# Performance work log

Hardware: AMD Instinct MI355X
Metric: run time of the kernel (lower is better)

## Reference

```python
import jax, jax.numpy as jnp
import numpy as np

N_ADDR = 400000
N_TX = 400000
E = 1500000
F_IN = 64
HID = 32
OUT = 2


def _sage(x_src, x_dst, ei, Wl, bl, Wr, n_dst):
    # SAGEConv: mean-aggregate source feats over incoming edges, then
    # out = lin_l(agg) + lin_r(x_dst). Nodes with no in-edges get agg=0.
    src, dst = ei[0], ei[1]
    msg = x_src[src]                                            # [E, F]
    s = jax.ops.segment_sum(msg, dst, num_segments=n_dst)       # [N_dst, F]
    cnt = jax.ops.segment_sum(jnp.ones((ei.shape[1], 1), x_src.dtype), dst,
                              num_segments=n_dst)               # [N_dst, 1]
    agg = s / jnp.maximum(cnt, 1.0)
    return agg @ Wl + bl + x_dst @ Wr


def setup_inputs() -> dict:
    key = jax.random.key(0)
    ks = jax.random.split(key, 24)
    d = {}
    d['x_addr'] = jax.random.normal(ks[0], (N_ADDR, F_IN), jnp.float32)
    d['x_tx'] = jax.random.normal(ks[1], (N_TX, F_IN), jnp.float32)
    d['ei_at'] = jax.random.randint(ks[2], (2, E), 0, N_ADDR)   # addr->tx (src idx < N_ADDR, dst idx < N_TX)
    d['ei_ta'] = jax.random.randint(ks[3], (2, E), 0, N_TX)     # tx->addr
    def w(k, i, o):
        return jax.random.normal(k, (i, o), jnp.float32) * (1.0 / np.sqrt(i))
    d['w1_tx_l'] = w(ks[4], F_IN, HID); d['b1_tx'] = jnp.zeros((HID,), jnp.float32)
    d['w1_tx_r'] = w(ks[5], F_IN, HID)
    d['w1_ad_l'] = w(ks[6], F_IN, HID); d['b1_ad'] = jnp.zeros((HID,), jnp.float32)
    d['w1_ad_r'] = w(ks[7], F_IN, HID)
    d['w2_tx_l'] = w(ks[8], HID, HID); d['b2_tx'] = jnp.zeros((HID,), jnp.float32)
    d['w2_tx_r'] = w(ks[9], HID, HID)
    d['w2_ad_l'] = w(ks[10], HID, HID); d['b2_ad'] = jnp.zeros((HID,), jnp.float32)
    d['w2_ad_r'] = w(ks[11], HID, HID)
    d['w3_tx_l'] = w(ks[12], HID, HID); d['b3_tx'] = jnp.zeros((HID,), jnp.float32)
    d['w3_tx_r'] = w(ks[13], HID, HID)
    d['w3_ad_l'] = w(ks[14], HID, HID); d['b3_ad'] = jnp.zeros((HID,), jnp.float32)
    d['w3_ad_r'] = w(ks[15], HID, HID)
    d['w_out'] = w(ks[16], HID, OUT); d['b_out'] = jnp.zeros((OUT,), jnp.float32)
    return d


def reference(x_addr, x_tx, ei_at, ei_ta,
              w1_tx_l, b1_tx, w1_tx_r, w1_ad_l, b1_ad, w1_ad_r,
              w2_tx_l, b2_tx, w2_tx_r, w2_ad_l, b2_ad, w2_ad_r,
              w3_tx_l, b3_tx, w3_tx_r, w3_ad_l, b3_ad, w3_ad_r,
              w_out, b_out):
    # Layer 1 (both node types updated simultaneously from previous x_dict)
    tx = jax.nn.relu(_sage(x_addr, x_tx, ei_at, w1_tx_l, b1_tx, w1_tx_r, N_TX))
    ad = jax.nn.relu(_sage(x_tx, x_addr, ei_ta, w1_ad_l, b1_ad, w1_ad_r, N_ADDR))
    # Layer 2
    tx2 = jax.nn.relu(_sage(ad, tx, ei_at, w2_tx_l, b2_tx, w2_tx_r, N_TX))
    ad2 = jax.nn.relu(_sage(tx, ad, ei_ta, w2_ad_l, b2_ad, w2_ad_r, N_ADDR))
    # Layer 3
    ad3 = jax.nn.relu(_sage(tx2, ad2, ei_ta, w3_ad_l, b3_ad, w3_ad_r, N_ADDR))
    # Final classifier on 'addr' nodes (dropout is identity at inference)
    return ad3 @ w_out + b_out
```

## Files before the change

### kernel.cpp

```cpp
#include <hip/hip_runtime.h>

#define NADDR 400000
#define NTX   400000
#define NEDGE 1500000
#define FIN   64
#define HID   32
#define NB    1563
#define LSTR  36

static inline int cdiv_host(long a, int b) { return (int)((a + b - 1) / b); }


__global__ void k_hist(const int* __restrict__ at_dst, const int* __restrict__ ta_dst,
                       int* __restrict__ bcnt , int GH) {
    __shared__ int h[NB];
    bool wh = blockIdx.x >= GH;
    int blk = blockIdx.x - (wh ? GH : 0);
    const int* dst = wh ? ta_dst : at_dst;
    for (int i = threadIdx.x; i < NB; i += 256) h[i] = 0;
    __syncthreads();
    for (long e = (long)blk * 256 + threadIdx.x; e < NEDGE; e += (long)GH * 256)
        atomicAdd(&h[dst[e] >> 8], 1);
    __syncthreads();
    int* g = bcnt + (wh ? NB : 0);
    for (int i = threadIdx.x; i < NB; i += 256) {
        int v = h[i];
        if (v) atomicAdd(&g[i], v);
    }
}

__global__ void k_scan_nb(const int* __restrict__ bcnt, int* __restrict__ bbase,
                          int* __restrict__ gcur) {
    __shared__ int sm[256];
    __shared__ int carry;
    int w = blockIdx.x;
    int t = threadIdx.x;
    if (t == 0) carry = 0;
    __syncthreads();
    for (int base = 0; base < NB; base += 256) {
        int i = base + t;
        int v = (i < NB) ? bcnt[w * NB + i] : 0;
        sm[t] = v;
        __syncthreads();
        for (int off = 1; off < 256; off <<= 1) {
            int x = (t >= off) ? sm[t - off] : 0;
            __syncthreads();
            sm[t] += x;
            __syncthreads();
        }
        int excl = sm[t] - v + carry;
        if (i < NB) { bbase[w * (NB + 1) + i] = excl; gcur[w * NB + i] = excl; }
        int tot = sm[255];
        __syncthreads();
        if (t == 0) carry += tot;
        __syncthreads();
    }
    if (t == 0) bbase[w * (NB + 1) + NB] = NEDGE;
}

__global__ void k_dist(const int* __restrict__ ei_at, const int* __restrict__ ei_ta,
                       int* __restrict__ gcur, unsigned* __restrict__ eb_at,
                       unsigned* __restrict__ eb_ta, int GD) {
    __shared__ int h[NB];
    __shared__ int bs[NB];
    bool wh = blockIdx.x >= GD;
    int blk = blockIdx.x - (wh ? GD : 0);
    const int* ei = wh ? ei_ta : ei_at;
    unsigned* eb = wh ? eb_ta : eb_at;
    for (int i = threadIdx.x; i < NB; i += 256) h[i] = 0;
    __syncthreads();
    long e0 = (long)blk * 256 + threadIdx.x;
    long stride = (long)GD * 256;
    for (long e = e0; e < NEDGE; e += stride)
        atomicAdd(&h[ei[NEDGE + e] >> 8], 1);
    __syncthreads();
    int* gc = gcur + (wh ? NB : 0);
    for (int i = threadIdx.x; i < NB; i += 256) {
        int c = h[i];
        bs[i] = c ? atomicAdd(&gc[i], c) : 0;
        h[i] = 0;
    }
    __syncthreads();
    for (long e = e0; e < NEDGE; e += stride) {
        int d = ei[NEDGE + e];
        int s = ei[e];
        int b = d >> 8;
        int r = atomicAdd(&h[b], 1);
        eb[bs[b] + r] = ((unsigned)s << 8) | (unsigned)(d & 255);
    }
}

__global__ void k_csrb(const unsigned* __restrict__ eb_at, const unsigned* __restrict__ eb_ta,
                       const int* __restrict__ bbase,
                       int* __restrict__ rp_tx, int* __restrict__ rp_ad,
                       int* __restrict__ col_at, int* __restrict__ col_ta) {
    __shared__ int deg[256];
    __shared__ int cur[256];
    __shared__ int sm[256];
    bool wh = blockIdx.x >= NB;
    int b = blockIdx.x - (wh ? NB : 0);
    const unsigned* eb = wh ? eb_ta : eb_at;
    int* rp  = wh ? rp_ad  : rp_tx;
    int* col = wh ? col_ta : col_at;
    const int* bb = bbase + (wh ? (NB + 1) : 0);
    int e0 = bb[b], e1 = bb[b + 1];
    int t = threadIdx.x;
    deg[t] = 0;
    __syncthreads();
    for (int e = e0 + t; e < e1; e += 256)
        atomicAdd(&deg[eb[e] & 255], 1);
    __syncthreads();
    int v = deg[t];
    sm[t] = v;
    __syncthreads();
    for (int off = 1; off < 256; off <<= 1) {
        int x = (t >= off) ? sm[t - off] : 0;
        __syncthreads();
        sm[t] += x;
        __syncthreads();
    }
    int excl = sm[t] - v;
    int node = b * 256 + t;
    if (node < 400000) rp[node] = e0 + excl;
    cur[t] = e0 + excl;
    __syncthreads();
    for (int e = e0 + t; e < e1; e += 256) {
        unsigned p = eb[e];
        int idx = atomicAdd(&cur[p & 255], 1);
        col[idx] = (int)(p >> 8);
    }
    if (t == 0 && b == 0) rp[400000] = NEDGE;
}

template<int F, bool DUAL>
__global__ __launch_bounds__(256)
void k_pre(const float* __restrict__ x,
           const float* __restrict__ wa, const float* __restrict__ ba,
           float* __restrict__ outa,
           const float* __restrict__ wb, const float* __restrict__ bb,
           float* __restrict__ outb, int n) {
    __shared__ alignas(16) float xs[256 * LSTR];
    int t = threadIdx.x;
    long row0 = (long)blockIdx.x * 256;

    float aa[HID], ab[DUAL ? HID : 1];
#pragma unroll
    for (int j = 0; j < HID; ++j) aa[j] = ba ? ba[j] : 0.0f;
    if (DUAL) {
#pragma unroll
        for (int j = 0; j < HID; ++j) ab[j] = bb[j];
    }

    for (int kt = 0; kt < F / 32; ++kt) {
#pragma unroll
        for (int sub = 0; sub < 8; ++sub) {
            int f = sub * 256 + t;
            int r = f >> 3, k4 = f & 7;
            long gr = row0 + r;
            if (gr >= n) gr = n - 1;
            float4 v = *(const float4*)(x + gr * F + kt * 32 + k4 * 4);
            *(float4*)(&xs[r * LSTR + k4 * 4]) = v;
        }
        __syncthreads();
        float xr[32];
#pragma unroll
        for (int q = 0; q < 8; ++q) {
            float4 v = *(const float4*)(&xs[t * LSTR + q * 4]);
            xr[q * 4 + 0] = v.x; xr[q * 4 + 1] = v.y;
            xr[q * 4 + 2] = v.z; xr[q * 4 + 3] = v.w;
        }
        const float* wka = wa + kt * 32 * HID;
#pragma unroll
        for (int k = 0; k < 32; ++k) {
            float xk = xr[k];
            const float* wr = wka + k * HID;
#pragma unroll
            for (int j = 0; j < HID; ++j) aa[j] = __builtin_fmaf(xk, wr[j], aa[j]);
        }
        if (DUAL) {
            const float* wkb = wb + kt * 32 * HID;
#pragma unroll
            for (int k = 0; k < 32; ++k) {
                float xk = xr[k];
                const float* wr = wkb + k * HID;
#pragma unroll
                for (int j = 0; j < HID; ++j) ab[j] = __builtin_fmaf(xk, wr[j], ab[j]);
            }
        }
        __syncthreads();
    }

#pragma unroll
    for (int j = 0; j < HID; j += 4)
        *(float4*)(&xs[t * LSTR + j]) = make_float4(aa[j], aa[j + 1], aa[j + 2], aa[j + 3]);
    __syncthreads();
#pragma unroll
    for (int sub = 0; sub < 8; ++sub) {
        int f = sub * 256 + t;
        int r = f >> 3, k4 = f & 7;
        long gr = row0 + r;
        if (gr < n) {
            float4 v = *(const float4*)(&xs[r * LSTR + k4 * 4]);
            *(float4*)(outa + gr * HID + k4 * 4) = v;
        }
    }
    if (DUAL) {
        __syncthreads();
#pragma unroll
        for (int j = 0; j < HID; j += 4)
            *(float4*)(&xs[t * LSTR + j]) = make_float4(ab[j], ab[j + 1], ab[j + 2], ab[j + 3]);
        __syncthreads();
#pragma unroll
        for (int sub = 0; sub < 8; ++sub) {
            int f = sub * 256 + t;
            int r = f >> 3, k4 = f & 7;
            long gr = row0 + r;
            if (gr < n) {
                float4 v = *(const float4*)(&xs[r * LSTR + k4 * 4]);
                *(float4*)(outb + gr * HID + k4 * 4) = v;
            }
        }
    }
}

template<bool FINAL>
__global__ __launch_bounds__(256)
void k_agg(const int* __restrict__ rp, const int* __restrict__ col,
           const float* __restrict__ preL, const float* __restrict__ preR,
           float* __restrict__ y,
           const float* __restrict__ wo, const float* __restrict__ bo, int n) {
    int t = blockIdx.x * 256 + threadIdx.x;
    int g = t >> 3;
    int u = t & 7;
    if (g >= n) return;
    int p0 = rp[g], p1 = rp[g + 1];

    float ax = 0.0f, ay = 0.0f, az = 0.0f, aw = 0.0f;
    for (int k = p0; k < p1; k += 8) {
        int last = p1 - 1;
        int idx[8];
#pragma unroll
        for (int q = 0; q < 8; ++q) {
            int e = k + q;
            idx[q] = col[e < p1 ? e : last];
        }
        float4 v[8];
#pragma unroll
        for (int q = 0; q < 8; ++q)
            v[q] = *(const float4*)(preL + (size_t)idx[q] * HID + u * 4);
#pragma unroll
        for (int q = 0; q < 8; ++q) {
            if (k + q < p1) {
                ax += v[q].x; ay += v[q].y; az += v[q].z; aw += v[q].w;
            }
        }
    }
    float inv = 1.0f / fmaxf((float)(p1 - p0), 1.0f);
    float4 r = *(const float4*)(preR + (size_t)g * HID + u * 4);
    float4 h;
    h.x = fmaxf(__builtin_fmaf(ax, inv, r.x), 0.0f);
    h.y = fmaxf(__builtin_fmaf(ay, inv, r.y), 0.0f);
    h.z = fmaxf(__builtin_fmaf(az, inv, r.z), 0.0f);
    h.w = fmaxf(__builtin_fmaf(aw, inv, r.w), 0.0f);

    if (!FINAL) {
        *(float4*)(y + (size_t)g * HID + u * 4) = h;
    } else {
        int j = u * 4;
        float o0 = h.x * wo[(j + 0) * 2 + 0] + h.y * wo[(j + 1) * 2 + 0]
                 + h.z * wo[(j + 2) * 2 + 0] + h.w * wo[(j + 3) * 2 + 0];
        float o1 = h.x * wo[(j + 0) * 2 + 1] + h.y * wo[(j + 1) * 2 + 1]
                 + h.z * wo[(j + 2) * 2 + 1] + h.w * wo[(j + 3) * 2 + 1];
#pragma unroll
        for (int m = 4; m >= 1; m >>= 1) {
            o0 += __shfl_xor(o0, m, 8);
            o1 += __shfl_xor(o1, m, 8);
        }
        if (u == 0) {
            y[(size_t)g * 2 + 0] = o0 + bo[0];
            y[(size_t)g * 2 + 1] = o1 + bo[1];
        }
    }
}


extern "C" void kernel_launch(void* const* d_in, const int* in_sizes, int n_in,
                              void* d_out, int out_size, void* d_ws, size_t ws_size,
                              hipStream_t stream) {
    const float* x_addr  = (const float*)d_in[0];
    const float* x_tx    = (const float*)d_in[1];
    const int*   ei_at   = (const int*)d_in[2];
    const int*   ei_ta   = (const int*)d_in[3];
    const float* w1_tx_l = (const float*)d_in[4];  const float* b1_tx = (const float*)d_in[5];
    const float* w1_tx_r = (const float*)d_in[6];
    const float* w1_ad_l = (const float*)d_in[7];  const float* b1_ad = (const float*)d_in[8];
    const float* w1_ad_r = (const float*)d_in[9];
    const float* w2_tx_l = (const float*)d_in[10]; const float* b2_tx = (const float*)d_in[11];
    const float* w2_tx_r = (const float*)d_in[12];
    const float* w2_ad_l = (const float*)d_in[13]; const float* b2_ad = (const float*)d_in[14];
    const float* w2_ad_r = (const float*)d_in[15];
    const float* w3_ad_l = (const float*)d_in[19]; const float* b3_ad = (const float*)d_in[20];
    const float* w3_ad_r = (const float*)d_in[21];
    const float* w_out   = (const float*)d_in[22]; const float* b_out = (const float*)d_in[23];
    float* out = (float*)d_out;

    char* base = (char*)d_ws;
    int* bcnt   = (int*)base;  base += (size_t)(2 * NB) * 4;
    int* bbase  = (int*)base;  base += (size_t)(2 * (NB + 1)) * 4;
    int* gcur   = (int*)base;  base += (size_t)(2 * NB) * 4;
    int* rp_tx  = (int*)base;  base += (size_t)(NTX + 1) * 4;
    int* rp_ad  = (int*)base;  base += (size_t)(NADDR + 1) * 4;
    int* col_at = (int*)base;  base += (size_t)NEDGE * 4;
    int* col_ta = (int*)base;  base += (size_t)NEDGE * 4;
    unsigned* eb_at = (unsigned*)base;  base += (size_t)NEDGE * 4;
    unsigned* eb_ta = (unsigned*)base;  base += (size_t)NEDGE * 4;
    base = (char*)(((size_t)base + 255) & ~(size_t)255);
    const size_t SLOT = (size_t)400000 * HID;
    float* A = (float*)base;
    float* B = A + SLOT;
    float* C = B + SLOT;
    float* D = C + SLOT;

    dim3 blk(256);
    int gN = cdiv_host(400000, 256);
    int gG = cdiv_host((long)400000 * 8, 256);
    const int GH = 96, GD = 192;

    hipMemsetAsync(bcnt, 0, (size_t)(2 * NB) * 4, stream);
    k_hist<<<2 * GH, blk, 0, stream>>>(ei_at + NEDGE, ei_ta + NEDGE, bcnt, GH);
    k_scan_nb<<<2, blk, 0, stream>>>(bcnt, bbase, gcur);
    k_dist<<<2 * GD, blk, 0, stream>>>(ei_at, ei_ta, gcur, eb_at, eb_ta, GD);
    k_csrb<<<2 * NB, blk, 0, stream>>>(eb_at, eb_ta, bbase, rp_tx, rp_ad, col_at, col_ta);

    k_pre<FIN, true><<<gN, blk, 0, stream>>>(x_addr, w1_tx_l, nullptr, A,
                                             w1_ad_r, b1_ad, B, NADDR);
    k_pre<FIN, true><<<gN, blk, 0, stream>>>(x_tx, w1_ad_l, nullptr, C,
                                             w1_tx_r, b1_tx, D, NTX);
    k_agg<false><<<gG, blk, 0, stream>>>(rp_tx, col_at, A, D, D, nullptr, nullptr, NTX);
    k_agg<false><<<gG, blk, 0, stream>>>(rp_ad, col_ta, C, B, B, nullptr, nullptr, NADDR);

    k_pre<HID, true><<<gN, blk, 0, stream>>>(D, w2_ad_l, nullptr, A,
                                             w2_tx_r, b2_tx, C, NTX);
    k_pre<HID, true><<<gN, blk, 0, stream>>>(B, w2_tx_l, nullptr, B,
                                             w2_ad_r, b2_ad, D, NADDR);
    k_agg<false><<<gG, blk, 0, stream>>>(rp_tx, col_at, B, C, C, nullptr, nullptr, NTX);
    k_agg<false><<<gG, blk, 0, stream>>>(rp_ad, col_ta, A, D, D, nullptr, nullptr, NADDR);

    k_pre<HID, false><<<gN, blk, 0, stream>>>(C, w3_ad_l, nullptr, A,
                                              nullptr, nullptr, nullptr, NTX);
    k_pre<HID, false><<<gN, blk, 0, stream>>>(D, w3_ad_r, b3_ad, B,
                                              nullptr, nullptr, nullptr, NADDR);
    k_agg<true><<<gG, blk, 0, stream>>>(rp_ad, col_ta, A, B, out, w_out, b_out, NADDR);
}
```

Baseline: 659.5 us.

## Use column-major intermediates and two-rows-per-thread projection kernels

The dual-output projection kernel is replaced by a single-output kernel that computes two rows per thread on 128-thread blocks, so each weight load feeds two FMAs. Layer outputs from the aggregation are now written column-major, which lets the layer-2/3 projections read features with coalesced scalar loads and no shared-memory staging. The edge-bucket scratch is aliased with a new feature buffer to save workspace. In exchange there are more kernel launches, the scattered column-major stores in aggregation are uncoalesced, and register pressure is higher with 64 accumulators per thread.

Result: slower. 811.6 us (+23.1%).

```diff
diff --git a/kernel.cpp b/kernel.cpp
--- a/kernel.cpp
+++ b/kernel.cpp
@@ -7,6 +7,8 @@
 #define HID   32
 #define NB    1563
 #define LSTR  36
+#define NND   400000
+#define NHALF 200000
 
 static inline int cdiv_host(long a, int b) { return (int)((a + b - 1) / b); }
 
@@ -121,7 +123,7 @@
     }
     int excl = sm[t] - v;
     int node = b * 256 + t;
-    if (node < 400000) rp[node] = e0 + excl;
+    if (node < NND) rp[node] = e0 + excl;
     cur[t] = e0 + excl;
     __syncthreads();
     for (int e = e0 + t; e < e1; e += 256) {
@@ -129,101 +131,101 @@
         int idx = atomicAdd(&cur[p & 255], 1);
         col[idx] = (int)(p >> 8);
     }
-    if (t == 0 && b == 0) rp[400000] = NEDGE;
-}
-
-template<int F, bool DUAL>
-__global__ __launch_bounds__(256)
-void k_pre(const float* __restrict__ x,
-           const float* __restrict__ wa, const float* __restrict__ ba,
-           float* __restrict__ outa,
-           const float* __restrict__ wb, const float* __restrict__ bb,
-           float* __restrict__ outb, int n) {
+    if (t == 0 && b == 0) rp[NND] = NEDGE;
+}
+
+template<int F>
+__global__ __launch_bounds__(128, 2)
+void k_preS(const float* __restrict__ x, const float* __restrict__ w,
+            const float* __restrict__ b, float* __restrict__ out, int n) {
     __shared__ alignas(16) float xs[256 * LSTR];
     int t = threadIdx.x;
     long row0 = (long)blockIdx.x * 256;
 
-    float aa[HID], ab[DUAL ? HID : 1];
-#pragma unroll
-    for (int j = 0; j < HID; ++j) aa[j] = ba ? ba[j] : 0.0f;
-    if (DUAL) {
-#pragma unroll
-        for (int j = 0; j < HID; ++j) ab[j] = bb[j];
-    }
+    float a0[HID], a1[HID];
+#pragma unroll
+    for (int j = 0; j < HID; ++j) { float bv = b ? b[j] : 0.0f; a0[j] = bv; a1[j] = bv; }
 
     for (int kt = 0; kt < F / 32; ++kt) {
-#pragma unroll
-        for (int sub = 0; sub < 8; ++sub) {
-            int f = sub * 256 + t;
+        if (kt) __syncthreads();
+#pragma unroll
+        for (int sub = 0; sub < 16; ++sub) {
+            int f = sub * 128 + t;
             int r = f >> 3, k4 = f & 7;
             long gr = row0 + r;
             if (gr >= n) gr = n - 1;
-            float4 v = *(const float4*)(x + gr * F + kt * 32 + k4 * 4);
-            *(float4*)(&xs[r * LSTR + k4 * 4]) = v;
-        }
-        __syncthreads();
-        float xr[32];
+            *(float4*)(&xs[r * LSTR + k4 * 4]) = *(const float4*)(x + gr * F + kt * 32 + k4 * 4);
+        }
+        __syncthreads();
+        float xA[32], xB[32];
 #pragma unroll
         for (int q = 0; q < 8; ++q) {
             float4 v = *(const float4*)(&xs[t * LSTR + q * 4]);
-            xr[q * 4 + 0] = v.x; xr[q * 4 + 1] = v.y;
-            xr[q * 4 + 2] = v.z; xr[q * 4 + 3] = v.w;
-        }
-        const float* wka = wa + kt * 32 * HID;
+            xA[q * 4] = v.x; xA[q * 4 + 1] = v.y; xA[q * 4 + 2] = v.z; xA[q * 4 + 3] = v.w;
+            float4 u = *(const float4*)(&xs[(t + 128) * LSTR + q * 4]);
+            xB[q * 4] = u.x; xB[q * 4 + 1] = u.y; xB[q * 4 + 2] = u.z; xB[q * 4 + 3] = u.w;
+        }
+        const float* wk = w + kt * 32 * HID;
 #pragma unroll
         for (int k = 0; k < 32; ++k) {
-            float xk = xr[k];
-            const float* wr = wka + k * HID;
-#pragma unroll
-            for (int j = 0; j < HID; ++j) aa[j] = __builtin_fmaf(xk, wr[j], aa[j]);
-        }
-        if (DUAL) {
-            const float* wkb = wb + kt * 32 * HID;
-#pragma unroll
-            for (int k = 0; k < 32; ++k) {
-                float xk = xr[k];
-                const float* wr = wkb + k * HID;
-#pragma unroll
-                for (int j = 0; j < HID; ++j) ab[j] = __builtin_fmaf(xk, wr[j], ab[j]);
+            float f0 = xA[k], f1 = xB[k];
+            const float* wr = wk + k * HID;
+#pragma unroll
+            for (int j = 0; j < HID; ++j) {
+                float wv = wr[j];
+                a0[j] = __builtin_fmaf(f0, wv, a0[j]);
+                a1[j] = __builtin_fmaf(f1, wv, a1[j]);
             }
         }
-        __syncthreads();
-    }
-
-#pragma unroll
-    for (int j = 0; j < HID; j += 4)
-        *(float4*)(&xs[t * LSTR + j]) = make_float4(aa[j], aa[j + 1], aa[j + 2], aa[j + 3]);
-    __syncthreads();
-#pragma unroll
-    for (int sub = 0; sub < 8; ++sub) {
-        int f = sub * 256 + t;
+    }
+
+    __syncthreads();
+#pragma unroll
+    for (int j = 0; j < HID; j += 4) {
+        *(float4*)(&xs[t * LSTR + j]) = make_float4(a0[j], a0[j + 1], a0[j + 2], a0[j + 3]);
+        *(float4*)(&xs[(t + 128) * LSTR + j]) = make_float4(a1[j], a1[j + 1], a1[j + 2], a1[j + 3]);
+    }
+    __syncthreads();
+#pragma unroll
+    for (int sub = 0; sub < 16; ++sub) {
+        int f = sub * 128 + t;
         int r = f >> 3, k4 = f & 7;
         long gr = row0 + r;
-        if (gr < n) {
-            float4 v = *(const float4*)(&xs[r * LSTR + k4 * 4]);
-            *(float4*)(outa + gr * HID + k4 * 4) = v;
-        }
-    }
-    if (DUAL) {
-        __syncthreads();
-#pragma unroll
-        for (int j = 0; j < HID; j += 4)
-            *(float4*)(&xs[t * LSTR + j]) = make_float4(ab[j], ab[j + 1], ab[j + 2], ab[j + 3]);
-        __syncthreads();
-#pragma unroll
-        for (int sub = 0; sub < 8; ++sub) {
-            int f = sub * 256 + t;
-            int r = f >> 3, k4 = f & 7;
-            long gr = row0 + r;
-            if (gr < n) {
-                float4 v = *(const float4*)(&xs[r * LSTR + k4 * 4]);
-                *(float4*)(outb + gr * HID + k4 * 4) = v;
-            }
-        }
-    }
-}
-
-template<bool FINAL>
+        if (gr < n)
+            *(float4*)(out + gr * HID + k4 * 4) = *(const float4*)(&xs[r * LSTR + k4 * 4]);
+    }
+}
+
+__global__ __launch_bounds__(256, 2)
+void k_preCM(const float* __restrict__ xT, const float* __restrict__ w,
+             const float* __restrict__ b, float* __restrict__ out) {
+    int i = blockIdx.x * 256 + threadIdx.x;
+    if (i >= NHALF) return;
+    float a0[HID], a1[HID];
+#pragma unroll
+    for (int j = 0; j < HID; ++j) { float bv = b ? b[j] : 0.0f; a0[j] = bv; a1[j] = bv; }
+#pragma unroll
+    for (int k = 0; k < 32; ++k) {
+        float f0 = xT[(size_t)k * NND + i];
+        float f1 = xT[(size_t)k * NND + i + NHALF];
+        const float* wr = w + k * HID;
+#pragma unroll
+        for (int j = 0; j < HID; ++j) {
+            float wv = wr[j];
+            a0[j] = __builtin_fmaf(f0, wv, a0[j]);
+            a1[j] = __builtin_fmaf(f1, wv, a1[j]);
+        }
+    }
+    float* o0 = out + (size_t)i * HID;
+    float* o1 = out + (size_t)(i + NHALF) * HID;
+#pragma unroll
+    for (int j = 0; j < HID; j += 4) {
+        *(float4*)(o0 + j) = make_float4(a0[j], a0[j + 1], a0[j + 2], a0[j + 3]);
+        *(float4*)(o1 + j) = make_float4(a1[j], a1[j + 1], a1[j + 2], a1[j + 3]);
+    }
+}
+
+template<bool CM, bool FINAL>
 __global__ __launch_bounds__(256)
 void k_agg(const int* __restrict__ rp, const int* __restrict__ col,
            const float* __restrict__ preL, const float* __restrict__ preR,
@@ -263,9 +265,7 @@
     h.z = fmaxf(__builtin_fmaf(az, inv, r.z), 0.0f);
     h.w = fmaxf(__builtin_fmaf(aw, inv, r.w), 0.0f);
 
-    if (!FINAL) {
-        *(float4*)(y + (size_t)g * HID + u * 4) = h;
-    } else {
+    if (FINAL) {
         int j = u * 4;
         float o0 = h.x * wo[(j + 0) * 2 + 0] + h.y * wo[(j + 1) * 2 + 0]
                  + h.z * wo[(j + 2) * 2 + 0] + h.w * wo[(j + 3) * 2 + 0];
@@ -280,6 +280,14 @@
             y[(size_t)g * 2 + 0] = o0 + bo[0];
             y[(size_t)g * 2 + 1] = o1 + bo[1];
         }
+    } else if (CM) {
+        int c = u * 4;
+        y[(size_t)(c + 0) * NND + g] = h.x;
+        y[(size_t)(c + 1) * NND + g] = h.y;
+        y[(size_t)(c + 2) * NND + g] = h.z;
+        y[(size_t)(c + 3) * NND + g] = h.w;
+    } else {
+        *(float4*)(y + (size_t)g * HID + u * 4) = h;
     }
 }
 
@@ -308,22 +316,25 @@
     int* bcnt   = (int*)base;  base += (size_t)(2 * NB) * 4;
     int* bbase  = (int*)base;  base += (size_t)(2 * (NB + 1)) * 4;
     int* gcur   = (int*)base;  base += (size_t)(2 * NB) * 4;
-    int* rp_tx  = (int*)base;  base += (size_t)(NTX + 1) * 4;
-    int* rp_ad  = (int*)base;  base += (size_t)(NADDR + 1) * 4;
+    int* rp_tx  = (int*)base;  base += (size_t)(NND + 1) * 4;
+    int* rp_ad  = (int*)base;  base += (size_t)(NND + 1) * 4;
     int* col_at = (int*)base;  base += (size_t)NEDGE * 4;
     int* col_ta = (int*)base;  base += (size_t)NEDGE * 4;
-    unsigned* eb_at = (unsigned*)base;  base += (size_t)NEDGE * 4;
-    unsigned* eb_ta = (unsigned*)base;  base += (size_t)NEDGE * 4;
     base = (char*)(((size_t)base + 255) & ~(size_t)255);
-    const size_t SLOT = (size_t)400000 * HID;
-    float* A = (float*)base;
+    const size_t SLOT = (size_t)NND * HID;
+    float* E = (float*)base;
+    unsigned* eb_at = (unsigned*)base;
+    unsigned* eb_ta = eb_at + (size_t)NEDGE;
+    float* A = E + SLOT;
     float* B = A + SLOT;
     float* C = B + SLOT;
     float* D = C + SLOT;
 
     dim3 blk(256);
-    int gN = cdiv_host(400000, 256);
-    int gG = cdiv_host((long)400000 * 8, 256);
+    dim3 blk128(128);
+    int gN  = cdiv_host(NND, 256);
+    int gCM = cdiv_host(NHALF, 256);
+    int gG  = cdiv_host((long)NND * 8, 256);
     const int GH = 96, GD = 192;
 
     hipMemsetAsync(bcnt, 0, (size_t)(2 * NB) * 4, stream);
@@ -332,23 +343,21 @@
     k_dist<<<2 * GD, blk, 0, stream>>>(ei_at, ei_ta, gcur, eb_at, eb_ta, GD);
     k_csrb<<<2 * NB, blk, 0, stream>>>(eb_at, eb_ta, bbase, rp_tx, rp_ad, col_at, col_ta);
 
-    k_pre<FIN, true><<<gN, blk, 0, stream>>>(x_addr, w1_tx_l, nullptr, A,
-                                             w1_ad_r, b1_ad, B, NADDR);
-    k_pre<FIN, true><<<gN, blk, 0, stream>>>(x_tx, w1_ad_l, nullptr, C,
-                                             w1_tx_r, b1_tx, D, NTX);
-    k_agg<false><<<gG, blk, 0, stream>>>(rp_tx, col_at, A, D, D, nullptr, nullptr, NTX);
-    k_agg<false><<<gG, blk, 0, stream>>>(rp_ad, col_ta, C, B, B, nullptr, nullptr, NADDR);
-
-    k_pre<HID, true><<<gN, blk, 0, stream>>>(D, w2_ad_l, nullptr, A,
-                                             w2_tx_r, b2_tx, C, NTX);
-    k_pre<HID, true><<<gN, blk, 0, stream>>>(B, w2_tx_l, nullptr, B,
-                                             w2_ad_r, b2_ad, D, NADDR);
-    k_agg<false><<<gG, blk, 0, stream>>>(rp_tx, col_at, B, C, C, nullptr, nullptr, NTX);
-    k_agg<false><<<gG, blk, 0, stream>>>(rp_ad, col_ta, A, D, D, nullptr, nullptr, NADDR);
-
-    k_pre<HID, false><<<gN, blk, 0, stream>>>(C, w3_ad_l, nullptr, A,
-                                              nullptr, nullptr, nullptr, NTX);
-    k_pre<HID, false><<<gN, blk, 0, stream>>>(D, w3_ad_r, b3_ad, B,
-                                              nullptr, nullptr, nullptr, NADDR);
-    k_agg<true><<<gG, blk, 0, stream>>>(rp_ad, col_ta, A, B, out, w_out, b_out, NADDR);
-}
+    k_preS<FIN><<<gN, blk128, 0, stream>>>(x_addr, w1_tx_l, nullptr, A, NADDR);
+    k_preS<FIN><<<gN, blk128, 0, stream>>>(x_tx, w1_tx_r, b1_tx, D, NTX);
+    k_agg<true, false><<<gG, blk, 0, stream>>>(rp_tx, col_at, A, D, C, nullptr, nullptr, NTX);
+    k_preS<FIN><<<gN, blk128, 0, stream>>>(x_tx, w1_ad_l, nullptr, A, NTX);
+    k_preS<FIN><<<gN, blk128, 0, stream>>>(x_addr, w1_ad_r, b1_ad, D, NADDR);
+    k_agg<true, false><<<gG, blk, 0, stream>>>(rp_ad, col_ta, A, D, B, nullptr, nullptr, NADDR);
+
+    k_preCM<<<gCM, blk, 0, stream>>>(B, w2_tx_l, nullptr, A);
+    k_preCM<<<gCM, blk, 0, stream>>>(C, w2_tx_r, b2_tx, D);
+    k_preCM<<<gCM, blk, 0, stream>>>(C, w2_ad_l, nullptr, E);
+    k_agg<true, false><<<gG, blk, 0, stream>>>(rp_tx, col_at, A, D, C, nullptr, nullptr, NTX);
+    k_preCM<<<gCM, blk, 0, stream>>>(B, w2_ad_r, b2_ad, A);
+    k_agg<true, false><<<gG, blk, 0, stream>>>(rp_ad, col_ta, E, A, D, nullptr, nullptr, NADDR);
+
+    k_preCM<<<gCM, blk, 0, stream>>>(C, w3_ad_l, nullptr, A);
+    k_preCM<<<gCM, blk, 0, stream>>>(D, w3_ad_r, b3_ad, B);
+    k_agg<false, true><<<gG, blk, 0, stream>>>(rp_ad, col_ta, A, B, out, w_out, b_out, NADDR);
+}
```
